# Kernel tuning notes

Measured on AMD Instinct MI355X. Metric: run time of the kernel, lower is better.

Reference implementation:

```python
import jax, jax.numpy as jnp
import numpy as np

N_NODES = 50000
N_EDGES = 1000000


def _edge_conv(x, src, dst, W, b, n_nodes):
    """PyG EdgeConv: msg = nn(cat([x_i, x_j - x_i])), aggr=max over incoming edges."""
    xi = x[dst]                      # [E, C] target features
    xj = x[src]                      # [E, C] source features
    m = jnp.concatenate([xi, xj - xi], axis=-1)          # [E, 2C]
    m = jax.nn.relu(m @ W + b)                           # [E, C_out]
    out = jax.ops.segment_max(m, dst, num_segments=n_nodes)  # [N, C_out]
    # empty segments produce -inf; PyG fills with 0
    return jnp.where(jnp.isfinite(out), out, 0.0)


def setup_inputs() -> dict:
    key = jax.random.key(0)
    ks = jax.random.split(key, 12)
    x = jax.random.normal(ks[0], (N_NODES, 3), dtype=jnp.float32)
    edge_index = jax.random.randint(ks[1], (2, N_EDGES), 0, N_NODES, dtype=jnp.int64)

    def lin(k, fan_in, fan_out):
        s = 1.0 / np.sqrt(fan_in)
        kw, kb = jax.random.split(k)
        W = jax.random.uniform(kw, (fan_in, fan_out), jnp.float32, -s, s)
        b = jax.random.uniform(kb, (fan_out,), jnp.float32, -s, s)
        return W, b

    W1, b1 = lin(ks[2], 6, 64)       # conv1 MLP([3*2, 64])
    W2, b2 = lin(ks[3], 128, 128)    # conv2 MLP([64*2, 128])
    W3, b3 = lin(ks[4], 256, 512)    # conv3 MLP([128*2, 512])
    W4, b4 = lin(ks[5], 512, 256)    # lin1 MLP([512, 256])
    W5, b5 = lin(ks[6], 256, 3)      # lin1 final Linear(256, 3)
    return {"x": x, "edge_index": edge_index,
            "W1": W1, "b1": b1, "W2": W2, "b2": b2, "W3": W3, "b3": b3,
            "W4": W4, "b4": b4, "W5": W5, "b5": b5}


def reference(x, edge_index, W1, b1, W2, b2, W3, b3, W4, b4, W5, b5):
    src = edge_index[0]  # x_j
    dst = edge_index[1]  # x_i (aggregation target)
    n = x.shape[0]
    x1 = _edge_conv(x, src, dst, W1, b1, n)    # [N, 64]
    x2 = _edge_conv(x1, src, dst, W2, b2, n)   # [N, 128]
    x3 = _edge_conv(x2, src, dst, W3, b3, n)   # [N, 512]
    x4 = jax.nn.relu(x3 @ W4 + b4) @ W5 + b5   # [N, 3]
    return x + x4
```

## Files before the change

kernel.cpp:

```cpp
#include <hip/hip_runtime.h>
#include <hip/hip_bf16.h>

static constexpr int NN = 50000;
static constexpr int NE = 1000000;

typedef short bf16x8 __attribute__((ext_vector_type(8)));
typedef float f32x4 __attribute__((ext_vector_type(4)));

__device__ inline float bf2f_raw(unsigned short u) {
    return __uint_as_float(((unsigned int)u) << 16);
}
__device__ inline unsigned short f2bf(float f) {
    unsigned int u = __float_as_uint(f);
    u += 0x7fffu + ((u >> 16) & 1u);
    return (unsigned short)(u >> 16);
}


__global__ void hist_kernel(const int* __restrict__ dst, int* __restrict__ deg) {
    int e = blockIdx.x * blockDim.x + threadIdx.x;
    if (e < NE) atomicAdd(&deg[dst[e]], 1);
}

__global__ __launch_bounds__(1024) void scan_kernel(const int* __restrict__ deg,
                                                    int* __restrict__ rowstart) {
    __shared__ int wave_sums[16];
    __shared__ int carry_s;
    int tid = threadIdx.x;
    int lane = tid & 63;
    int wave = tid >> 6;
    if (tid == 0) carry_s = 0;
    __syncthreads();
    for (int base = 0; base < NN; base += 1024) {
        int idx = base + tid;
        int v = (idx < NN) ? deg[idx] : 0;
        int x = v;
        #pragma unroll
        for (int off = 1; off < 64; off <<= 1) {
            int y = __shfl_up(x, off);
            if (lane >= off) x += y;
        }
        if (lane == 63) wave_sums[wave] = x;
        __syncthreads();
        if (wave == 0 && lane < 16) {
            int s = wave_sums[lane];
            #pragma unroll
            for (int off = 1; off < 16; off <<= 1) {
                int y = __shfl_up(s, off);
                if (lane >= off) s += y;
            }
            wave_sums[lane] = s;
        }
        __syncthreads();
        int wave_off = wave ? wave_sums[wave - 1] : 0;
        int chunk_total = wave_sums[15];
        int carry = carry_s;
        if (idx < NN) rowstart[idx] = carry + wave_off + x - v;
        __syncthreads();
        if (tid == 0) carry_s = carry + chunk_total;
        __syncthreads();
    }
    if (tid == 0) rowstart[NN] = carry_s;
}

__global__ void scatter_kernel(const int* __restrict__ src, const int* __restrict__ dst,
                               const int* __restrict__ rowstart, int* __restrict__ cursor,
                               int* __restrict__ csr) {
    int e = blockIdx.x * blockDim.x + threadIdx.x;
    if (e < NE) {
        int d = dst[e];
        int pos = atomicAdd(&cursor[d], 1);
        csr[rowstart[d] + pos] = src[e];
    }
}


template<int CIN, int COUT>
__global__ void prep_split_t_kernel(const float* __restrict__ W,
                                    unsigned short* __restrict__ Wtbt,
                                    unsigned short* __restrict__ Wbt) {
    int t = blockIdx.x * blockDim.x + threadIdx.x;
    if (t >= CIN * COUT) return;
    int k = t / COUT, c = t % COUT;
    float wt = W[k * COUT + c];
    float wb = W[(CIN + k) * COUT + c];
    Wtbt[c * CIN + k] = f2bf(wt - wb);
    Wbt[c * CIN + k] = f2bf(wb);
}

template<int K, int N>
__global__ void prep_t_kernel(const float* __restrict__ W, unsigned short* __restrict__ Wt) {
    int t = blockIdx.x * blockDim.x + threadIdx.x;
    if (t >= K * N) return;
    int k = t / N, n = t % N;
    Wt[n * K + k] = f2bf(W[k * N + n]);
}


__global__ void conv1_s_kernel(const float* __restrict__ x, const float* __restrict__ W1,
                               unsigned short* __restrict__ s) {
    int t = blockIdx.x * blockDim.x + threadIdx.x;
    int i = t >> 6, c = t & 63;
    if (i >= NN) return;
    float v = x[i * 3 + 0] * W1[3 * 64 + c] + x[i * 3 + 1] * W1[4 * 64 + c] +
              x[i * 3 + 2] * W1[5 * 64 + c];
    s[t] = f2bf(v);
}

__global__ void conv1_x_kernel(const float* __restrict__ x, const float* __restrict__ W1,
                               const float* __restrict__ b1,
                               const unsigned short* __restrict__ t1,
                               unsigned short* __restrict__ x1) {
    int t = blockIdx.x * blockDim.x + threadIdx.x;
    int i = t >> 6, c = t & 63;
    if (i >= NN) return;
    float a = x[i * 3 + 0] * (W1[0 * 64 + c] - W1[3 * 64 + c]) +
              x[i * 3 + 1] * (W1[1 * 64 + c] - W1[4 * 64 + c]) +
              x[i * 3 + 2] * (W1[2 * 64 + c] - W1[5 * 64 + c]) + b1[c];
    float v = a + bf2f_raw(t1[t]);
    x1[t] = f2bf(fmaxf(v, 0.f));
}


template<int C>
__global__ void edge_max_kernel(const unsigned short* __restrict__ s,
                                const int* __restrict__ rowstart, const int* __restrict__ csr,
                                unsigned short* __restrict__ t) {
    int gt = blockIdx.x * blockDim.x + threadIdx.x;
    int i = gt / C, c = gt % C;
    if (i >= NN) return;
    int e0 = rowstart[i], e1 = rowstart[i + 1];
    float acc = -INFINITY;
    for (int e = e0; e < e1; ++e) {
        int j = csr[e];
        acc = fmaxf(acc, bf2f_raw(s[(size_t)j * C + c]));
    }
    t[gt] = f2bf(acc);
}


template<int C, int VEC>
__global__ __launch_bounds__(256) void edge_max_vec_kernel(
    const unsigned short* __restrict__ s, const int* __restrict__ rowstart,
    const int* __restrict__ csr, unsigned short* __restrict__ t) {
    int wid = (blockIdx.x * 256 + threadIdx.x) >> 6;
    int lane = threadIdx.x & 63;
    if (wid >= NN) return;
    int e0 = __builtin_amdgcn_readfirstlane(rowstart[wid]);
    int e1 = __builtin_amdgcn_readfirstlane(rowstart[wid + 1]);
    float acc[VEC];
    #pragma unroll
    for (int v = 0; v < VEC; ++v) acc[v] = -INFINITY;
    const unsigned short* sl = s + (size_t)lane * VEC;
    int nedge = e1 - e0;
    for (int base = 0; base < nedge; base += 64) {
        int rem = nedge - base;
        int myj = (lane < rem) ? csr[e0 + base + lane] : 0;
        int cnt = rem < 64 ? rem : 64;
        int q = 0;
        for (; q + 1 < cnt; q += 2) {
            int j0 = __shfl(myj, q);
            int j1 = __shfl(myj, q + 1);
            if constexpr (VEC == 8) {
                uint4 v0 = *(const uint4*)(sl + (size_t)j0 * C);
                uint4 v1 = *(const uint4*)(sl + (size_t)j1 * C);
                acc[0] = fmaxf(acc[0], bf2f_raw((unsigned short)(v0.x & 0xffff)));
                acc[1] = fmaxf(acc[1], bf2f_raw((unsigned short)(v0.x >> 16)));
                acc[2] = fmaxf(acc[2], bf2f_raw((unsigned short)(v0.y & 0xffff)));
                acc[3] = fmaxf(acc[3], bf2f_raw((unsigned short)(v0.y >> 16)));
                acc[4] = fmaxf(acc[4], bf2f_raw((unsigned short)(v0.z & 0xffff)));
                acc[5] = fmaxf(acc[5], bf2f_raw((unsigned short)(v0.z >> 16)));
                acc[6] = fmaxf(acc[6], bf2f_raw((unsigned short)(v0.w & 0xffff)));
                acc[7] = fmaxf(acc[7], bf2f_raw((unsigned short)(v0.w >> 16)));
                acc[0] = fmaxf(acc[0], bf2f_raw((unsigned short)(v1.x & 0xffff)));
                acc[1] = fmaxf(acc[1], bf2f_raw((unsigned short)(v1.x >> 16)));
                acc[2] = fmaxf(acc[2], bf2f_raw((unsigned short)(v1.y & 0xffff)));
                acc[3] = fmaxf(acc[3], bf2f_raw((unsigned short)(v1.y >> 16)));
                acc[4] = fmaxf(acc[4], bf2f_raw((unsigned short)(v1.z & 0xffff)));
                acc[5] = fmaxf(acc[5], bf2f_raw((unsigned short)(v1.z >> 16)));
                acc[6] = fmaxf(acc[6], bf2f_raw((unsigned short)(v1.w & 0xffff)));
                acc[7] = fmaxf(acc[7], bf2f_raw((unsigned short)(v1.w >> 16)));
            } else {
                unsigned int v0 = *(const unsigned int*)(sl + (size_t)j0 * C);
                unsigned int v1 = *(const unsigned int*)(sl + (size_t)j1 * C);
                acc[0] = fmaxf(acc[0], bf2f_raw((unsigned short)(v0 & 0xffff)));
                acc[1] = fmaxf(acc[1], bf2f_raw((unsigned short)(v0 >> 16)));
                acc[0] = fmaxf(acc[0], bf2f_raw((unsigned short)(v1 & 0xffff)));
                acc[1] = fmaxf(acc[1], bf2f_raw((unsigned short)(v1 >> 16)));
            }
        }
        if (q < cnt) {
            int j0 = __shfl(myj, q);
            if constexpr (VEC == 8) {
                uint4 v0 = *(const uint4*)(sl + (size_t)j0 * C);
                acc[0] = fmaxf(acc[0], bf2f_raw((unsigned short)(v0.x & 0xffff)));
                acc[1] = fmaxf(acc[1], bf2f_raw((unsigned short)(v0.x >> 16)));
                acc[2] = fmaxf(acc[2], bf2f_raw((unsigned short)(v0.y & 0xffff)));
                acc[3] = fmaxf(acc[3], bf2f_raw((unsigned short)(v0.y >> 16)));
                acc[4] = fmaxf(acc[4], bf2f_raw((unsigned short)(v0.z & 0xffff)));
                acc[5] = fmaxf(acc[5], bf2f_raw((unsigned short)(v0.z >> 16)));
                acc[6] = fmaxf(acc[6], bf2f_raw((unsigned short)(v0.w & 0xffff)));
                acc[7] = fmaxf(acc[7], bf2f_raw((unsigned short)(v0.w >> 16)));
            } else {
                unsigned int v0 = *(const unsigned int*)(sl + (size_t)j0 * C);
                acc[0] = fmaxf(acc[0], bf2f_raw((unsigned short)(v0 & 0xffff)));
                acc[1] = fmaxf(acc[1], bf2f_raw((unsigned short)(v0 >> 16)));
            }
        }
    }
    unsigned short* tp = t + (size_t)wid * C + lane * VEC;
    if constexpr (VEC == 8) {
        uint4 o;
        o.x = (unsigned int)f2bf(acc[0]) | ((unsigned int)f2bf(acc[1]) << 16);
        o.y = (unsigned int)f2bf(acc[2]) | ((unsigned int)f2bf(acc[3]) << 16);
        o.z = (unsigned int)f2bf(acc[4]) | ((unsigned int)f2bf(acc[5]) << 16);
        o.w = (unsigned int)f2bf(acc[6]) | ((unsigned int)f2bf(acc[7]) << 16);
        *(uint4*)tp = o;
    } else {
        *(unsigned int*)tp = (unsigned int)f2bf(acc[0]) | ((unsigned int)f2bf(acc[1]) << 16);
    }
}


template<bool HAS_T, bool RELU>
__global__ __launch_bounds__(256) void mfma_gemm_kernel(
    const unsigned short* __restrict__ A, const unsigned short* __restrict__ Bt,
    const float* __restrict__ bias, const unsigned short* __restrict__ T,
    unsigned short* __restrict__ C, int M, int N, int K) {
    __shared__ __align__(16) unsigned short Asl[128 * 40];
    __shared__ __align__(16) unsigned short Bsl[128 * 40];
    int tid = threadIdx.x;
    int mbase = blockIdx.y * 128, nbase = blockIdx.x * 128;
    int wave = tid >> 6, lane = tid & 63;
    int wm = (wave >> 1) * 64, wn = (wave & 1) * 64;
    int quad = lane >> 4, l16 = lane & 15;
    f32x4 acc[4][4] = {};
    for (int kb = 0; kb < K; kb += 32) {
        #pragma unroll
        for (int h = 0; h < 2; ++h) {
            int c = tid + h * 256;
            int r = c >> 2, kk = (c & 3) * 8;
            uint4 va = make_uint4(0u, 0u, 0u, 0u);
            int gr = mbase + r;
            if (gr < M) va = *(const uint4*)&A[(size_t)gr * K + kb + kk];
            *(uint4*)&Asl[r * 40 + kk] = va;
            uint4 vb = *(const uint4*)&Bt[(size_t)(nbase + r) * K + kb + kk];
            *(uint4*)&Bsl[r * 40 + kk] = vb;
        }
        __syncthreads();
        bf16x8 af[4], bfr[4];
        #pragma unroll
        for (int tt = 0; tt < 4; ++tt) {
            af[tt]  = *(const bf16x8*)&Asl[(wm + tt * 16 + l16) * 40 + quad * 8];
            bfr[tt] = *(const bf16x8*)&Bsl[(wn + tt * 16 + l16) * 40 + quad * 8];
        }
        #pragma unroll
        for (int mt = 0; mt < 4; ++mt)
            #pragma unroll
            for (int nt = 0; nt < 4; ++nt)
                acc[mt][nt] = __builtin_amdgcn_mfma_f32_16x16x32_bf16(
                    af[mt], bfr[nt], acc[mt][nt], 0, 0, 0);
        __syncthreads();
    }
    #pragma unroll
    for (int mt = 0; mt < 4; ++mt) {
        #pragma unroll
        for (int r = 0; r < 4; ++r) {
            int row = mbase + wm + mt * 16 + quad * 4 + r;
            if (row >= M) continue;
            #pragma unroll
            for (int nt = 0; nt < 4; ++nt) {
                int col = nbase + wn + nt * 16 + l16;
                float v = acc[mt][nt][r];
                if (bias) v += bias[col];
                if (HAS_T) v += bf2f_raw(T[(size_t)row * N + col]);
                if (RELU) v = fmaxf(v, 0.f);
                C[(size_t)row * N + col] = f2bf(v);
            }
        }
    }
}


__global__ void final_kernel(const unsigned short* __restrict__ h4,
                             const float* __restrict__ W5, const float* __restrict__ b5,
                             const float* __restrict__ x, float* __restrict__ out) {
    int gt = blockIdx.x * blockDim.x + threadIdx.x;
    int node = gt >> 6;
    int lane = gt & 63;
    if (node >= NN) return;
    ushort4 hv = ((const ushort4*)(h4 + (size_t)node * 256))[lane];
    float hj[4] = {bf2f_raw(hv.x), bf2f_raw(hv.y), bf2f_raw(hv.z), bf2f_raw(hv.w)};
    float acc0 = 0.f, acc1 = 0.f, acc2 = 0.f;
    #pragma unroll
    for (int j = 0; j < 4; ++j) {
        int k = lane * 4 + j;
        acc0 += hj[j] * W5[k * 3 + 0];
        acc1 += hj[j] * W5[k * 3 + 1];
        acc2 += hj[j] * W5[k * 3 + 2];
    }
    #pragma unroll
    for (int off = 32; off; off >>= 1) {
        acc0 += __shfl_down(acc0, off);
        acc1 += __shfl_down(acc1, off);
        acc2 += __shfl_down(acc2, off);
    }
    if (lane == 0) {
        out[node * 3 + 0] = x[node * 3 + 0] + acc0 + b5[0];
        out[node * 3 + 1] = x[node * 3 + 1] + acc1 + b5[1];
        out[node * 3 + 2] = x[node * 3 + 2] + acc2 + b5[2];
    }
}

__global__ void fallback_copy_kernel(const float* __restrict__ x, float* __restrict__ out) {
    int t = blockIdx.x * blockDim.x + threadIdx.x;
    if (t < NN * 3) out[t] = x[t];
}


extern "C" void kernel_launch(void* const* d_in, const int* in_sizes, int n_in,
                              void* d_out, int out_size, void* d_ws, size_t ws_size,
                              hipStream_t stream) {
    const float* x  = (const float*)d_in[0];
    const int*   ei = (const int*)d_in[1];
    const float* W1 = (const float*)d_in[2];
    const float* b1 = (const float*)d_in[3];
    const float* W2 = (const float*)d_in[4];
    const float* b2 = (const float*)d_in[5];
    const float* W3 = (const float*)d_in[6];
    const float* b3 = (const float*)d_in[7];
    const float* W4 = (const float*)d_in[8];
    const float* b4 = (const float*)d_in[9];
    const float* W5 = (const float*)d_in[10];
    const float* b5 = (const float*)d_in[11];
    float* out = (float*)d_out;

    char* p = (char*)d_ws;
    auto alloc = [&](size_t bytes) -> void* {
        void* r = (void*)p;
        p += (bytes + 255) & ~(size_t)255;
        return r;
    };
    int* deg      = (int*)alloc((size_t)NN * 4);
    int* rowstart = (int*)alloc((size_t)(NN + 1) * 4);
    int* cursor   = (int*)alloc((size_t)NN * 4);
    int* csr      = (int*)alloc((size_t)NE * 4);
    unsigned short* Wtb2t = (unsigned short*)alloc(128 * 64 * 2);
    unsigned short* Wb2t  = (unsigned short*)alloc(128 * 64 * 2);
    unsigned short* Wtb3t = (unsigned short*)alloc(512 * 128 * 2);
    unsigned short* Wb3t  = (unsigned short*)alloc(512 * 128 * 2);
    unsigned short* W4t   = (unsigned short*)alloc(256 * 512 * 2);
    unsigned short* x1     = (unsigned short*)alloc((size_t)NN * 64 * 2);
    unsigned short* x2     = (unsigned short*)alloc((size_t)NN * 128 * 2);
    unsigned short* s_slab = (unsigned short*)alloc((size_t)NN * 512 * 2);
    unsigned short* t_slab = (unsigned short*)alloc((size_t)NN * 512 * 2);
    size_t need = (size_t)(p - (char*)d_ws);
    if (ws_size < need) {
        fallback_copy_kernel<<<(NN * 3 + 255) / 256, 256, 0, stream>>>(x, out);
        return;
    }
    unsigned short* x3 = s_slab;
    unsigned short* h4 = t_slab;

    const int* src = ei;
    const int* dst = ei + NE;

    hipMemsetAsync(deg, 0, (size_t)NN * 4, stream);
    hipMemsetAsync(cursor, 0, (size_t)NN * 4, stream);
    hist_kernel<<<(NE + 255) / 256, 256, 0, stream>>>(dst, deg);
    scan_kernel<<<1, 1024, 0, stream>>>(deg, rowstart);
    scatter_kernel<<<(NE + 255) / 256, 256, 0, stream>>>(src, dst, rowstart, cursor, csr);

    prep_split_t_kernel<64, 128><<<32, 256, 0, stream>>>(W2, Wtb2t, Wb2t);
    prep_split_t_kernel<128, 512><<<256, 256, 0, stream>>>(W3, Wtb3t, Wb3t);
    prep_t_kernel<512, 256><<<512, 256, 0, stream>>>(W4, W4t);

    conv1_s_kernel<<<NN * 64 / 256, 256, 0, stream>>>(x, W1, s_slab);
    edge_max_kernel<64><<<NN * 64 / 256, 256, 0, stream>>>(s_slab, rowstart, csr, t_slab);
    conv1_x_kernel<<<NN * 64 / 256, 256, 0, stream>>>(x, W1, b1, t_slab, x1);

    mfma_gemm_kernel<false, false><<<dim3(1, 391), 256, 0, stream>>>(
        x1, Wb2t, nullptr, nullptr, s_slab, NN, 128, 64);
    edge_max_vec_kernel<128, 2><<<12500, 256, 0, stream>>>(s_slab, rowstart, csr, t_slab);
    mfma_gemm_kernel<true, true><<<dim3(1, 391), 256, 0, stream>>>(
        x1, Wtb2t, b2, t_slab, x2, NN, 128, 64);

    mfma_gemm_kernel<false, false><<<dim3(4, 391), 256, 0, stream>>>(
        x2, Wb3t, nullptr, nullptr, s_slab, NN, 512, 128);
    edge_max_vec_kernel<512, 8><<<12500, 256, 0, stream>>>(s_slab, rowstart, csr, t_slab);
    mfma_gemm_kernel<true, true><<<dim3(4, 391), 256, 0, stream>>>(
        x2, Wtb3t, b3, t_slab, x3, NN, 512, 128);

    mfma_gemm_kernel<false, true><<<dim3(2, 391), 256, 0, stream>>>(
        x3, W4t, b4, nullptr, h4, NN, 256, 512);

    final_kernel<<<NN / 4, 256, 0, stream>>>(h4, W5, b5, x, out);
}
```

Measured before the change: 700.9 us.

## Fuse EdgeConv node GEMMs into one wide GEMM and fold add-relu into edge max

```diff
diff --git a/kernel.cpp b/kernel.cpp
--- a/kernel.cpp
+++ b/kernel.cpp
@@ -1,5 +1,4 @@
 #include <hip/hip_runtime.h>
-#include <hip/hip_bf16.h>
 
 static constexpr int NN = 50000;
 static constexpr int NE = 1000000;
@@ -14,6 +13,18 @@
     unsigned int u = __float_as_uint(f);
     u += 0x7fffu + ((u >> 16) & 1u);
     return (unsigned short)(u >> 16);
+}
+__device__ inline void fmax2(float& a0, float& a1, unsigned int v) {
+    a0 = fmaxf(a0, bf2f_raw((unsigned short)(v & 0xffffu)));
+    a1 = fmaxf(a1, bf2f_raw((unsigned short)(v >> 16)));
+}
+__device__ inline unsigned int pack2(float f0, float f1) {
+    return (unsigned int)f2bf(f0) | ((unsigned int)f2bf(f1) << 16);
+}
+__device__ inline unsigned int addrelu2(unsigned int a, float t0, float t1) {
+    float f0 = fmaxf(bf2f_raw((unsigned short)(a & 0xffffu)) + t0, 0.f);
+    float f1 = fmaxf(bf2f_raw((unsigned short)(a >> 16)) + t1, 0.f);
+    return pack2(f0, f1);
 }
 
 
@@ -107,125 +118,139 @@
     s[t] = f2bf(v);
 }
 
-__global__ void conv1_x_kernel(const float* __restrict__ x, const float* __restrict__ W1,
-                               const float* __restrict__ b1,
-                               const unsigned short* __restrict__ t1,
-                               unsigned short* __restrict__ x1) {
-    int t = blockIdx.x * blockDim.x + threadIdx.x;
-    int i = t >> 6, c = t & 63;
-    if (i >= NN) return;
-    float a = x[i * 3 + 0] * (W1[0 * 64 + c] - W1[3 * 64 + c]) +
-              x[i * 3 + 1] * (W1[1 * 64 + c] - W1[4 * 64 + c]) +
-              x[i * 3 + 2] * (W1[2 * 64 + c] - W1[5 * 64 + c]) + b1[c];
-    float v = a + bf2f_raw(t1[t]);
-    x1[t] = f2bf(fmaxf(v, 0.f));
-}
-
-
-template<int C>
-__global__ void edge_max_kernel(const unsigned short* __restrict__ s,
-                                const int* __restrict__ rowstart, const int* __restrict__ csr,
-                                unsigned short* __restrict__ t) {
-    int gt = blockIdx.x * blockDim.x + threadIdx.x;
-    int i = gt / C, c = gt % C;
-    if (i >= NN) return;
-    int e0 = rowstart[i], e1 = rowstart[i + 1];
-    float acc = -INFINITY;
-    for (int e = e0; e < e1; ++e) {
-        int j = csr[e];
-        acc = fmaxf(acc, bf2f_raw(s[(size_t)j * C + c]));
-    }
-    t[gt] = f2bf(acc);
-}
-
-
-template<int C, int VEC>
-__global__ __launch_bounds__(256) void edge_max_vec_kernel(
-    const unsigned short* __restrict__ s, const int* __restrict__ rowstart,
-    const int* __restrict__ csr, unsigned short* __restrict__ t) {
+
+__global__ __launch_bounds__(256) void edge_fused_conv1_kernel(
+    const unsigned short* __restrict__ s1, const int* __restrict__ rowstart,
+    const int* __restrict__ csr, const float* __restrict__ x,
+    const float* __restrict__ W1, const float* __restrict__ b1,
+    unsigned short* __restrict__ x1) {
     int wid = (blockIdx.x * 256 + threadIdx.x) >> 6;
     int lane = threadIdx.x & 63;
     if (wid >= NN) return;
     int e0 = __builtin_amdgcn_readfirstlane(rowstart[wid]);
     int e1 = __builtin_amdgcn_readfirstlane(rowstart[wid + 1]);
-    float acc[VEC];
-    #pragma unroll
-    for (int v = 0; v < VEC; ++v) acc[v] = -INFINITY;
-    const unsigned short* sl = s + (size_t)lane * VEC;
+    int h = lane >> 5, c0 = (lane & 31) * 2;
+    float t0 = -INFINITY, t1 = -INFINITY;
+    const unsigned short* sb = s1 + c0;
     int nedge = e1 - e0;
     for (int base = 0; base < nedge; base += 64) {
         int rem = nedge - base;
-        int myj = (lane < rem) ? csr[e0 + base + lane] : 0;
+        int myj = csr[(lane < rem) ? (e0 + base + lane) : e0];
         int cnt = rem < 64 ? rem : 64;
-        int q = 0;
-        for (; q + 1 < cnt; q += 2) {
-            int j0 = __shfl(myj, q);
-            int j1 = __shfl(myj, q + 1);
-            if constexpr (VEC == 8) {
-                uint4 v0 = *(const uint4*)(sl + (size_t)j0 * C);
-                uint4 v1 = *(const uint4*)(sl + (size_t)j1 * C);
-                acc[0] = fmaxf(acc[0], bf2f_raw((unsigned short)(v0.x & 0xffff)));
-                acc[1] = fmaxf(acc[1], bf2f_raw((unsigned short)(v0.x >> 16)));
-                acc[2] = fmaxf(acc[2], bf2f_raw((unsigned short)(v0.y & 0xffff)));
-                acc[3] = fmaxf(acc[3], bf2f_raw((unsigned short)(v0.y >> 16)));
-                acc[4] = fmaxf(acc[4], bf2f_raw((unsigned short)(v0.z & 0xffff)));
-                acc[5] = fmaxf(acc[5], bf2f_raw((unsigned short)(v0.z >> 16)));
-                acc[6] = fmaxf(acc[6], bf2f_raw((unsigned short)(v0.w & 0xffff)));
-                acc[7] = fmaxf(acc[7], bf2f_raw((unsigned short)(v0.w >> 16)));
-                acc[0] = fmaxf(acc[0], bf2f_raw((unsigned short)(v1.x & 0xffff)));
-                acc[1] = fmaxf(acc[1], bf2f_raw((unsigned short)(v1.x >> 16)));
-                acc[2] = fmaxf(acc[2], bf2f_raw((unsigned short)(v1.y & 0xffff)));
-                acc[3] = fmaxf(acc[3], bf2f_raw((unsigned short)(v1.y >> 16)));
-                acc[4] = fmaxf(acc[4], bf2f_raw((unsigned short)(v1.z & 0xffff)));
-                acc[5] = fmaxf(acc[5], bf2f_raw((unsigned short)(v1.z >> 16)));
-                acc[6] = fmaxf(acc[6], bf2f_raw((unsigned short)(v1.w & 0xffff)));
-                acc[7] = fmaxf(acc[7], bf2f_raw((unsigned short)(v1.w >> 16)));
-            } else {
-                unsigned int v0 = *(const unsigned int*)(sl + (size_t)j0 * C);
-                unsigned int v1 = *(const unsigned int*)(sl + (size_t)j1 * C);
-                acc[0] = fmaxf(acc[0], bf2f_raw((unsigned short)(v0 & 0xffff)));
-                acc[1] = fmaxf(acc[1], bf2f_raw((unsigned short)(v0 >> 16)));
-                acc[0] = fmaxf(acc[0], bf2f_raw((unsigned short)(v1 & 0xffff)));
-                acc[1] = fmaxf(acc[1], bf2f_raw((unsigned short)(v1 >> 16)));
-            }
-        }
-        if (q < cnt) {
-            int j0 = __shfl(myj, q);
-            if constexpr (VEC == 8) {
-                uint4 v0 = *(const uint4*)(sl + (size_t)j0 * C);
-                acc[0] = fmaxf(acc[0], bf2f_raw((unsigned short)(v0.x & 0xffff)));
-                acc[1] = fmaxf(acc[1], bf2f_raw((unsigned short)(v0.x >> 16)));
-                acc[2] = fmaxf(acc[2], bf2f_raw((unsigned short)(v0.y & 0xffff)));
-                acc[3] = fmaxf(acc[3], bf2f_raw((unsigned short)(v0.y >> 16)));
-                acc[4] = fmaxf(acc[4], bf2f_raw((unsigned short)(v0.z & 0xffff)));
-                acc[5] = fmaxf(acc[5], bf2f_raw((unsigned short)(v0.z >> 16)));
-                acc[6] = fmaxf(acc[6], bf2f_raw((unsigned short)(v0.w & 0xffff)));
-                acc[7] = fmaxf(acc[7], bf2f_raw((unsigned short)(v0.w >> 16)));
-            } else {
-                unsigned int v0 = *(const unsigned int*)(sl + (size_t)j0 * C);
-                acc[0] = fmaxf(acc[0], bf2f_raw((unsigned short)(v0 & 0xffff)));
-                acc[1] = fmaxf(acc[1], bf2f_raw((unsigned short)(v0 >> 16)));
-            }
-        }
-    }
-    unsigned short* tp = t + (size_t)wid * C + lane * VEC;
-    if constexpr (VEC == 8) {
-        uint4 o;
-        o.x = (unsigned int)f2bf(acc[0]) | ((unsigned int)f2bf(acc[1]) << 16);
-        o.y = (unsigned int)f2bf(acc[2]) | ((unsigned int)f2bf(acc[3]) << 16);
-        o.z = (unsigned int)f2bf(acc[4]) | ((unsigned int)f2bf(acc[5]) << 16);
-        o.w = (unsigned int)f2bf(acc[6]) | ((unsigned int)f2bf(acc[7]) << 16);
-        *(uint4*)tp = o;
-    } else {
-        *(unsigned int*)tp = (unsigned int)f2bf(acc[0]) | ((unsigned int)f2bf(acc[1]) << 16);
-    }
-}
-
-
-template<bool HAS_T, bool RELU>
+        int cp = (cnt + 7) & ~7;
+        for (int q = 0; q < cp; q += 8) {
+            int j0 = __shfl(myj, q + 0 + h);
+            int j1 = __shfl(myj, q + 2 + h);
+            int j2 = __shfl(myj, q + 4 + h);
+            int j3 = __shfl(myj, q + 6 + h);
+            unsigned int v0 = *(const unsigned int*)(sb + (size_t)j0 * 64);
+            unsigned int v1 = *(const unsigned int*)(sb + (size_t)j1 * 64);
+            unsigned int v2 = *(const unsigned int*)(sb + (size_t)j2 * 64);
+            unsigned int v3 = *(const unsigned int*)(sb + (size_t)j3 * 64);
+            fmax2(t0, t1, v0);
+            fmax2(t0, t1, v1);
+            fmax2(t0, t1, v2);
+            fmax2(t0, t1, v3);
+        }
+    }
+    t0 = fmaxf(t0, __shfl_xor(t0, 32));
+    t1 = fmaxf(t1, __shfl_xor(t1, 32));
+    if (h == 0) {
+        float x0 = x[wid * 3 + 0], xv1 = x[wid * 3 + 1], xv2 = x[wid * 3 + 2];
+        int c1 = c0 + 1;
+        float a0 = x0 * (W1[c0] - W1[192 + c0]) + xv1 * (W1[64 + c0] - W1[256 + c0]) +
+                   xv2 * (W1[128 + c0] - W1[320 + c0]) + b1[c0];
+        float a1 = x0 * (W1[c1] - W1[192 + c1]) + xv1 * (W1[64 + c1] - W1[256 + c1]) +
+                   xv2 * (W1[128 + c1] - W1[320 + c1]) + b1[c1];
+        *(unsigned int*)(x1 + (size_t)wid * 64 + c0) =
+            pack2(fmaxf(a0 + t0, 0.f), fmaxf(a1 + t1, 0.f));
+    }
+}
+
+
+__global__ __launch_bounds__(256) void edge_fused128_kernel(
+    const unsigned short* __restrict__ as, const int* __restrict__ rowstart,
+    const int* __restrict__ csr, unsigned short* __restrict__ xout) {
+    int wid = (blockIdx.x * 256 + threadIdx.x) >> 6;
+    int lane = threadIdx.x & 63;
+    if (wid >= NN) return;
+    int e0 = __builtin_amdgcn_readfirstlane(rowstart[wid]);
+    int e1 = __builtin_amdgcn_readfirstlane(rowstart[wid + 1]);
+    float t0 = -INFINITY, t1 = -INFINITY;
+    const unsigned short* sb = as + 128 + (size_t)lane * 2;
+    int nedge = e1 - e0;
+    for (int base = 0; base < nedge; base += 64) {
+        int rem = nedge - base;
+        int myj = csr[(lane < rem) ? (e0 + base + lane) : e0];
+        int cnt = rem < 64 ? rem : 64;
+        int cp = (cnt + 3) & ~3;
+        for (int q = 0; q < cp; q += 4) {
+            int j0 = __shfl(myj, q + 0), j1 = __shfl(myj, q + 1);
+            int j2 = __shfl(myj, q + 2), j3 = __shfl(myj, q + 3);
+            unsigned int v0 = *(const unsigned int*)(sb + (size_t)j0 * 256);
+            unsigned int v1 = *(const unsigned int*)(sb + (size_t)j1 * 256);
+            unsigned int v2 = *(const unsigned int*)(sb + (size_t)j2 * 256);
+            unsigned int v3 = *(const unsigned int*)(sb + (size_t)j3 * 256);
+            fmax2(t0, t1, v0);
+            fmax2(t0, t1, v1);
+            fmax2(t0, t1, v2);
+            fmax2(t0, t1, v3);
+        }
+    }
+    unsigned int av = *(const unsigned int*)(as + (size_t)wid * 256 + lane * 2);
+    *(unsigned int*)(xout + (size_t)wid * 128 + lane * 2) = addrelu2(av, t0, t1);
+}
+
+
+__global__ __launch_bounds__(256) void edge_fused512_kernel(
+    const unsigned short* __restrict__ as, const int* __restrict__ rowstart,
+    const int* __restrict__ csr, unsigned short* __restrict__ xout) {
+    int wid = (blockIdx.x * 256 + threadIdx.x) >> 6;
+    int lane = threadIdx.x & 63;
+    if (wid >= NN) return;
+    int e0 = __builtin_amdgcn_readfirstlane(rowstart[wid]);
+    int e1 = __builtin_amdgcn_readfirstlane(rowstart[wid + 1]);
+    float acc[8];
+    #pragma unroll
+    for (int v = 0; v < 8; ++v) acc[v] = -INFINITY;
+    const unsigned short* sb = as + 512 + (size_t)lane * 8;
+    int nedge = e1 - e0;
+    for (int base = 0; base < nedge; base += 64) {
+        int rem = nedge - base;
+        int myj = csr[(lane < rem) ? (e0 + base + lane) : e0];
+        int cnt = rem < 64 ? rem : 64;
+        int cp = (cnt + 3) & ~3;
+        for (int q = 0; q < cp; q += 4) {
+            int j0 = __shfl(myj, q + 0), j1 = __shfl(myj, q + 1);
+            int j2 = __shfl(myj, q + 2), j3 = __shfl(myj, q + 3);
+            uint4 v0 = *(const uint4*)(sb + (size_t)j0 * 1024);
+            uint4 v1 = *(const uint4*)(sb + (size_t)j1 * 1024);
+            uint4 v2 = *(const uint4*)(sb + (size_t)j2 * 1024);
+            uint4 v3 = *(const uint4*)(sb + (size_t)j3 * 1024);
+            fmax2(acc[0], acc[1], v0.x); fmax2(acc[2], acc[3], v0.y);
+            fmax2(acc[4], acc[5], v0.z); fmax2(acc[6], acc[7], v0.w);
+            fmax2(acc[0], acc[1], v1.x); fmax2(acc[2], acc[3], v1.y);
+            fmax2(acc[4], acc[5], v1.z); fmax2(acc[6], acc[7], v1.w);
+            fmax2(acc[0], acc[1], v2.x); fmax2(acc[2], acc[3], v2.y);
+            fmax2(acc[4], acc[5], v2.z); fmax2(acc[6], acc[7], v2.w);
+            fmax2(acc[0], acc[1], v3.x); fmax2(acc[2], acc[3], v3.y);
+            fmax2(acc[4], acc[5], v3.z); fmax2(acc[6], acc[7], v3.w);
+        }
+    }
+    uint4 av = *(const uint4*)(as + (size_t)wid * 1024 + lane * 8);
+    uint4 o;
+    o.x = addrelu2(av.x, acc[0], acc[1]);
+    o.y = addrelu2(av.y, acc[2], acc[3]);
+    o.z = addrelu2(av.z, acc[4], acc[5]);
+    o.w = addrelu2(av.w, acc[6], acc[7]);
+    *(uint4*)(xout + (size_t)wid * 512 + lane * 8) = o;
+}
+
+
+template<bool RELU>
 __global__ __launch_bounds__(256) void mfma_gemm_kernel(
     const unsigned short* __restrict__ A, const unsigned short* __restrict__ Bt,
-    const float* __restrict__ bias, const unsigned short* __restrict__ T,
+    const float* __restrict__ bias, int bias_n,
     unsigned short* __restrict__ C, int M, int N, int K) {
     __shared__ __align__(16) unsigned short Asl[128 * 40];
     __shared__ __align__(16) unsigned short Bsl[128 * 40];
@@ -272,8 +297,7 @@
             for (int nt = 0; nt < 4; ++nt) {
                 int col = nbase + wn + nt * 16 + l16;
                 float v = acc[mt][nt][r];
-                if (bias) v += bias[col];
-                if (HAS_T) v += bf2f_raw(T[(size_t)row * N + col]);
+                if (col < bias_n) v += bias[col];
                 if (RELU) v = fmaxf(v, 0.f);
                 C[(size_t)row * N + col] = f2bf(v);
             }
@@ -345,22 +369,20 @@
     int* rowstart = (int*)alloc((size_t)(NN + 1) * 4);
     int* cursor   = (int*)alloc((size_t)NN * 4);
     int* csr      = (int*)alloc((size_t)NE * 4);
-    unsigned short* Wtb2t = (unsigned short*)alloc(128 * 64 * 2);
-    unsigned short* Wb2t  = (unsigned short*)alloc(128 * 64 * 2);
-    unsigned short* Wtb3t = (unsigned short*)alloc(512 * 128 * 2);
-    unsigned short* Wb3t  = (unsigned short*)alloc(512 * 128 * 2);
-    unsigned short* W4t   = (unsigned short*)alloc(256 * 512 * 2);
-    unsigned short* x1     = (unsigned short*)alloc((size_t)NN * 64 * 2);
-    unsigned short* x2     = (unsigned short*)alloc((size_t)NN * 128 * 2);
-    unsigned short* s_slab = (unsigned short*)alloc((size_t)NN * 512 * 2);
-    unsigned short* t_slab = (unsigned short*)alloc((size_t)NN * 512 * 2);
+    unsigned short* Bt2 = (unsigned short*)alloc(256 * 64 * 2);
+    unsigned short* Bt3 = (unsigned short*)alloc(1024 * 128 * 2);
+    unsigned short* W4t = (unsigned short*)alloc(256 * 512 * 2);
+    unsigned short* x1 = (unsigned short*)alloc((size_t)NN * 64 * 2);
+    unsigned short* x2 = (unsigned short*)alloc((size_t)NN * 128 * 2);
+    unsigned short* x3 = (unsigned short*)alloc((size_t)NN * 512 * 2);
+    unsigned short* as_slab = (unsigned short*)alloc((size_t)NN * 1024 * 2);
     size_t need = (size_t)(p - (char*)d_ws);
     if (ws_size < need) {
         fallback_copy_kernel<<<(NN * 3 + 255) / 256, 256, 0, stream>>>(x, out);
         return;
     }
-    unsigned short* x3 = s_slab;
-    unsigned short* h4 = t_slab;
+    unsigned short* s1 = as_slab;
+    unsigned short* h4 = as_slab;
 
     const int* src = ei;
     const int* dst = ei + NE;
@@ -371,28 +393,23 @@
     scan_kernel<<<1, 1024, 0, stream>>>(deg, rowstart);
     scatter_kernel<<<(NE + 255) / 256, 256, 0, stream>>>(src, dst, rowstart, cursor, csr);
 
-    prep_split_t_kernel<64, 128><<<32, 256, 0, stream>>>(W2, Wtb2t, Wb2t);
-    prep_split_t_kernel<128, 512><<<256, 256, 0, stream>>>(W3, Wtb3t, Wb3t);
+    prep_split_t_kernel<64, 128><<<32, 256, 0, stream>>>(W2, Bt2, Bt2 + 128 * 64);
+    prep_split_t_kernel<128, 512><<<256, 256, 0, stream>>>(W3, Bt3, Bt3 + 512 * 128);
     prep_t_kernel<512, 256><<<512, 256, 0, stream>>>(W4, W4t);
 
-    conv1_s_kernel<<<NN * 64 / 256, 256, 0, stream>>>(x, W1, s_slab);
-    edge_max_kernel<64><<<NN * 64 / 256, 256, 0, stream>>>(s_slab, rowstart, csr, t_slab);
-    conv1_x_kernel<<<NN * 64 / 256, 256, 0, stream>>>(x, W1, b1, t_slab, x1);
-
-    mfma_gemm_kernel<false, false><<<dim3(1, 391), 256, 0, stream>>>(
-        x1, Wb2t, nullptr, nullptr, s_slab, NN, 128, 64);
-    edge_max_vec_kernel<128, 2><<<12500, 256, 0, stream>>>(s_slab, rowstart, csr, t_slab);
-    mfma_gemm_kernel<true, true><<<dim3(1, 391), 256, 0, stream>>>(
-        x1, Wtb2t, b2, t_slab, x2, NN, 128, 64);
-
-    mfma_gemm_kernel<false, false><<<dim3(4, 391), 256, 0, stream>>>(
-        x2, Wb3t, nullptr, nullptr, s_slab, NN, 512, 128);
-    edge_max_vec_kernel<512, 8><<<12500, 256, 0, stream>>>(s_slab, rowstart, csr, t_slab);
-    mfma_gemm_kernel<true, true><<<dim3(4, 391), 256, 0, stream>>>(
-        x2, Wtb3t, b3, t_slab, x3, NN, 512, 128);
-
-    mfma_gemm_kernel<false, true><<<dim3(2, 391), 256, 0, stream>>>(
-        x3, W4t, b4, nullptr, h4, NN, 256, 512);
+    conv1_s_kernel<<<NN * 64 / 256, 256, 0, stream>>>(x, W1, s1);
+    edge_fused_conv1_kernel<<<12500, 256, 0, stream>>>(s1, rowstart, csr, x, W1, b1, x1);
+
+    mfma_gemm_kernel<false><<<dim3(2, 391), 256, 0, stream>>>(
+        x1, Bt2, b2, 128, as_slab, NN, 256, 64);
+    edge_fused128_kernel<<<12500, 256, 0, stream>>>(as_slab, rowstart, csr, x2);
+
+    mfma_gemm_kernel<false><<<dim3(8, 391), 256, 0, stream>>>(
+        x2, Bt3, b3, 512, as_slab, NN, 1024, 128);
+    edge_fused512_kernel<<<12500, 256, 0, stream>>>(as_slab, rowstart, csr, x3);
+
+    mfma_gemm_kernel<true><<<dim3(2, 391), 256, 0, stream>>>(
+        x3, W4t, b4, 256, h4, NN, 256, 512);
 
     final_kernel<<<NN / 4, 256, 0, stream>>>(h4, W5, b5, x, out);
 }
```

Result: faster. 630.2 us (-10.1%).
